# Kernel tuning notes

Measured on AMD Instinct MI355X. Metric: run time of the kernel, lower is better.

## Reference

```python
import jax, jax.numpy as jnp
import numpy as np

B, T, D = 8, 2048, 512
F = 512          # filters (== D due to residual add)
K = 7            # kernel_size
H = 128          # hidden_dim of kernel generator (hard-coded in source)
LN_EPS = 1e-3    # keras LayerNormalization default epsilon


def setup_inputs() -> dict:
    key = jax.random.key(0)
    ks = jax.random.split(key, 8)
    x = jax.random.normal(ks[0], (B, T, D), dtype=jnp.float32)
    # kernel generator: Dense(D->H, relu) then Dense(H->K*F)
    W1 = jax.random.normal(ks[1], (D, H), dtype=jnp.float32) * (1.0 / np.sqrt(D))
    b1 = jnp.zeros((H,), dtype=jnp.float32)
    W2 = jax.random.normal(ks[2], (H, K * F), dtype=jnp.float32) * (1.0 / np.sqrt(H))
    b2 = jnp.zeros((K * F,), dtype=jnp.float32)
    # LayerNorm params
    gamma = jnp.ones((F,), dtype=jnp.float32)
    beta = jnp.zeros((F,), dtype=jnp.float32)
    return {"x": x, "W1": W1, "b1": b1, "W2": W2, "b2": b2,
            "gamma": gamma, "beta": beta}


def _dynamic_conv_block(x, W1, b1, W2, b2, gamma, beta):
    # per-token dynamic kernels: [B, T, K, F]
    h = jax.nn.relu(jnp.einsum("btd,dh->bth", x, W1) + b1)
    kernels = (jnp.einsum("bth,hf->btf", h, W2) + b2).reshape(B, T, K, F)
    # extract sliding-window patches (same padding): [B, T, K, D]
    pad = K // 2
    xp = jnp.pad(x, ((0, 0), (pad, pad), (0, 0)))
    patches = jnp.stack([xp[:, i:i + T, :] for i in range(K)], axis=2)
    # per-token conv: contract over window K and input channels D
    conv_out = jnp.einsum("btkd,btkf->btf", patches, kernels)
    # residual + LayerNorm + relu (dropout is identity at inference)
    y = conv_out + x
    mu = jnp.mean(y, axis=-1, keepdims=True)
    var = jnp.mean(jnp.square(y - mu), axis=-1, keepdims=True)
    y = (y - mu) * jax.lax.rsqrt(var + LN_EPS) * gamma + beta
    return jax.nn.relu(y)


def reference(x, W1, b1, W2, b2, gamma, beta):
    return _dynamic_conv_block(x, W1, b1, W2, b2, gamma, beta)
```

## Files before the change

### kernel.cpp

```cpp
#include <hip/hip_runtime.h>

#define NT 2048
#define ND 512
#define NH 128
#define NKW 7
#define KP 960

typedef float f32x4 __attribute__((ext_vector_type(4)));
typedef __bf16 bf16x8 __attribute__((ext_vector_type(8)));
typedef unsigned short u16;
typedef unsigned int u32;
typedef u16 u16x8 __attribute__((ext_vector_type(8)));

__device__ __forceinline__ u16 f2bf(float f){
  u32 u = __builtin_bit_cast(u32, f);
  return (u16)((u + 0x7fffu + ((u>>16)&1u)) >> 16);
}
__device__ __forceinline__ float bf2f(u16 s){
  u32 u = ((u32)s)<<16;
  return __builtin_bit_cast(float, u);
}
__device__ __forceinline__ void store16_lds(void* p, const u16 u[8]){
  u32 d0 = (u32)u[0] | ((u32)u[1]<<16);
  u32 d1 = (u32)u[2] | ((u32)u[3]<<16);
  u32 d2 = (u32)u[4] | ((u32)u[5]<<16);
  u32 d3 = (u32)u[6] | ((u32)u[7]<<16);
  int4 vv; vv.x=(int)d0; vv.y=(int)d1; vv.z=(int)d2; vv.w=(int)d3;
  *(int4*)p = vv;
}

__global__ __launch_bounds__(256) void prep_kernel(
    const float* __restrict__ W1, const float* __restrict__ W2,
    const float* __restrict__ b2, u16* __restrict__ W1T, u16* __restrict__ B2T)
{
  __shared__ float T[64][65];
  const int b = blockIdx.x, tid = threadIdx.x;
  if (b < 16){
    const int d0 = (b>>1)*64, h0 = (b&1)*64;
    #pragma unroll
    for (int r=0;r<16;++r){
      int idx=r*256+tid; int dl=idx>>6, hl=idx&63;
      T[dl][hl] = W1[(size_t)(d0+dl)*NH + h0+hl];
    }
    __syncthreads();
    #pragma unroll
    for (int r=0;r<16;++r){
      int idx=r*256+tid; int hl=idx>>6, dl=idx&63;
      W1T[(size_t)(h0+hl)*ND + d0+dl] = f2bf(T[dl][hl]);
    }
  } else if (b < 128){
    const int bb = b-16;
    const int h0 = (bb&1)*64, c0 = (bb>>1)*64;
    #pragma unroll
    for (int r=0;r<16;++r){
      int idx=r*256+tid; int hl=idx>>6, cl=idx&63;
      T[hl][cl] = W2[(size_t)(h0+hl)*(NKW*ND) + c0+cl];
    }
    __syncthreads();
    #pragma unroll
    for (int r=0;r<16;++r){
      int idx=r*256+tid; int cl=idx>>6, hl=idx&63;
      int c = c0+cl; int n = c & (ND-1), k = c >> 9;
      B2T[(size_t)n*KP + k*NH + h0+hl] = f2bf(T[hl][cl]);
    }
  } else {
    const int bb = b-128;
    #pragma unroll
    for (int r=0;r<16;++r){
      int idx = bb*4096 + r*256 + tid;
      int n = idx>>6, j = idx&63;
      B2T[(size_t)n*KP + 896 + j] = (j<NKW)? f2bf(b2[(size_t)j*ND+n]) : (u16)0;
    }
  }
}

__device__ __forceinline__ void loadB2(const char* B2T, int kc, int w, int l,
                                       bf16x8 (*bf)[4]){
  #pragma unroll
  for (int kk=0;kk<2;++kk)
    #pragma unroll
    for (int ni=0;ni<4;++ni){
      int rowB = w*64 + ni*16 + (l&15);
      bf[kk][ni] = *(const bf16x8*)(B2T + (size_t)rowB*(KP*2) + kc*128 + kk*64 + (l>>4)*16);
    }
}
__device__ __forceinline__ void loadB1(const char* W1T, int kc, int w, int l,
                                       bf16x8 (*bf)[2]){
  #pragma unroll
  for (int kk=0;kk<2;++kk)
    #pragma unroll
    for (int ni=0;ni<2;++ni){
      int rowB = w*32 + ni*16 + (l&15);
      bf[kk][ni] = *(const bf16x8*)(W1T + (size_t)rowB*(ND*2) + kc*128 + kk*64 + (l>>4)*16);
    }
}

__global__ __launch_bounds__(256,2) void gemm1_kernel(
    const float* __restrict__ x, const u16* __restrict__ W1T,
    const float* __restrict__ b1, u16* __restrict__ hout, float* __restrict__ rs)
{
  __shared__ __align__(16) u16 At[2][32*64];
  const int tid = threadIdx.x, w = tid>>6, l = tid&63;
  const int m_base = blockIdx.x*32;
  const int row = tid>>3, slot = tid&7;
  const float* xrow = x + (size_t)(m_base+row)*ND + slot*8;
  float rsum = 0.f;
  f32x4 acc[2][2] = {};
  bf16x8 bufA[2][2], bufB[2][2];

  auto stageA = [&](u16* dst, const float4& p0, const float4& p1){
    rsum += (p0.x+p0.y)+(p0.z+p0.w)+((p1.x+p1.y)+(p1.z+p1.w));
    u16 u[8] = {f2bf(p0.x),f2bf(p0.y),f2bf(p0.z),f2bf(p0.w),
                f2bf(p1.x),f2bf(p1.y),f2bf(p1.z),f2bf(p1.w)};
    int byte = row*128 + ((slot*16) ^ ((row&7)<<4));
    store16_lds((char*)dst + byte, u);
  };

  float4 c0 = *(const float4*)(xrow);
  float4 c1 = *(const float4*)(xrow+4);
  loadB1((const char*)W1T, 0, w, l, bufA);
  stageA(At[0], c0, c1);
  __syncthreads();

  #pragma unroll
  for (int kc=0;kc<8;++kc){
    bf16x8 (*bc)[2] = (kc&1)? bufB : bufA;
    bf16x8 (*bn)[2] = (kc&1)? bufA : bufB;
    float4 n0, n1;
    if (kc<7){
      n0 = *(const float4*)(xrow + (kc+1)*64);
      n1 = *(const float4*)(xrow + (kc+1)*64 + 4);
      loadB1((const char*)W1T, kc+1, w, l, bn);
    }
    const char* curA = (const char*)At[kc&1];
    #pragma unroll
    for (int kk=0;kk<2;++kk){
      bf16x8 af[2];
      #pragma unroll
      for (int mi=0;mi<2;++mi){
        int r2 = mi*16 + (l&15);
        int byte = r2*128 + (((kk*64)+((l>>4)*16)) ^ ((r2&7)<<4));
        af[mi] = *(const bf16x8*)(curA + byte);
      }
      #pragma unroll
      for (int mi=0;mi<2;++mi)
        #pragma unroll
        for (int ni=0;ni<2;++ni)
          acc[mi][ni] = __builtin_amdgcn_mfma_f32_16x16x32_bf16(af[mi], bc[kk][ni], acc[mi][ni],0,0,0);
    }
    if (kc<7){
      stageA(At[(kc&1)^1], n0, n1);
      __syncthreads();
    }
  }
  rsum += __shfl_xor(rsum,1);
  rsum += __shfl_xor(rsum,2);
  rsum += __shfl_xor(rsum,4);
  if ((tid&7)==0) rs[m_base+row] = rsum;
  #pragma unroll
  for (int ni=0;ni<2;++ni){
    int n = w*32 + ni*16 + (l&15);
    float bias = b1[n];
    #pragma unroll
    for (int mi=0;mi<2;++mi){
      #pragma unroll
      for (int r=0;r<4;++r){
        int m = mi*16 + (l>>4)*4 + r;
        float v = fmaxf(acc[mi][ni][r] + bias, 0.f);
        hout[(size_t)(m_base+m)*NH + n] = f2bf(v);
      }
    }
  }
}

__global__ __launch_bounds__(512,2) void gemm2_kernel(
    const float* __restrict__ x, const u16* __restrict__ hbuf,
    const u16* __restrict__ B2T, const float* __restrict__ rs,
    const float* __restrict__ gamma, const float* __restrict__ beta,
    float* __restrict__ out)
{
  __shared__ __align__(16) u16 At[2][64*64];
  __shared__ float s_lds[64][8];
  __shared__ float red_s[64][8], red_q[64][8];
  __shared__ float mu_lds[64], rstd_lds[64];

  const int tid = threadIdx.x, w = tid>>6, l = tid&63;
  const int m_base = blockIdx.x*64;
  const int row = tid>>3, slot = tid&7;

  {
    int rr = tid>>3, k = tid&7;
    float v = 0.f;
    if (k < NKW){
      int tg = m_base + rr;
      int ti = tg & (NT-1);
      int idx = ti + k - 3;
      if (idx >= 0 && idx < NT) v = rs[(tg & ~(NT-1)) + idx];
    }
    s_lds[rr][k] = v;
  }
  u16x8 hv_e = *(const u16x8*)(hbuf + (size_t)(m_base+row)*NH + slot*8);
  u16x8 hv_o = *(const u16x8*)(hbuf + (size_t)(m_base+row)*NH + 64 + slot*8);

  bf16x8 bufA[2][4], bufB[2][4];
  loadB2((const char*)B2T, 0, w, l, bufA);

  auto stageA = [&](u16* dst, int kc2){
    u16 u[8];
    if (kc2 < 14){
      float sv = s_lds[row][kc2>>1];
      u16x8 hv = (kc2&1)? hv_o : hv_e;
      #pragma unroll
      for (int j=0;j<8;++j) u[j] = f2bf(bf2f(hv[j])*sv);
    } else {
      #pragma unroll
      for (int j=0;j<8;++j){
        int e2 = slot*8+j;
        u[j] = (e2<NKW)? f2bf(s_lds[row][e2]) : (u16)0;
      }
    }
    int byte = row*128 + ((slot*16) ^ ((row&7)<<4));
    store16_lds((char*)dst + byte, u);
  };

  __syncthreads();
  stageA(At[0], 0);
  __syncthreads();

  f32x4 acc[4][4] = {};
  #pragma unroll
  for (int kc=0;kc<15;++kc){
    bf16x8 (*bc)[4] = (kc&1)? bufB : bufA;
    bf16x8 (*bn)[4] = (kc&1)? bufA : bufB;
    if (kc<14) loadB2((const char*)B2T, kc+1, w, l, bn);
    const char* curA = (const char*)At[kc&1];
    #pragma unroll
    for (int kk=0;kk<2;++kk){
      bf16x8 af[4];
      #pragma unroll
      for (int mi=0;mi<4;++mi){
        int r2 = mi*16 + (l&15);
        int byte = r2*128 + (((kk*64)+((l>>4)*16)) ^ ((r2&7)<<4));
        af[mi] = *(const bf16x8*)(curA + byte);
      }
      #pragma unroll
      for (int mi=0;mi<4;++mi)
        #pragma unroll
        for (int ni=0;ni<4;++ni)
          acc[mi][ni] = __builtin_amdgcn_mfma_f32_16x16x32_bf16(af[mi], bc[kk][ni], acc[mi][ni],0,0,0);
    }
    if (kc<14){
      stageA(At[(kc&1)^1], kc+1);
      __syncthreads();
    }
  }

  #pragma unroll
  for (int mi=0;mi<4;++mi){
    #pragma unroll
    for (int r=0;r<4;++r){
      int m = mi*16 + (l>>4)*4 + r;
      int tg = m_base + m;
      float ps=0.f, pq=0.f;
      #pragma unroll
      for (int ni=0;ni<4;++ni){
        int n = w*64 + ni*16 + (l&15);
        float v = acc[mi][ni][r] + x[(size_t)tg*ND + n];
        acc[mi][ni][r] = v;
        ps += v; pq += v*v;
      }
      #pragma unroll
      for (int msk=1; msk<16; msk<<=1){ ps += __shfl_xor(ps,msk); pq += __shfl_xor(pq,msk); }
      if ((l&15)==0){ red_s[m][w]=ps; red_q[m][w]=pq; }
    }
  }
  __syncthreads();
  if (tid < 64){
    float ssum=0.f, sq=0.f;
    #pragma unroll
    for (int ww=0; ww<8; ++ww){ ssum += red_s[tid][ww]; sq += red_q[tid][ww]; }
    float mu = ssum * (1.0f/ND);
    float var = sq*(1.0f/ND) - mu*mu;
    mu_lds[tid] = mu;
    rstd_lds[tid] = rsqrtf(var + 1e-3f);
  }
  __syncthreads();
  float gv[4], bv[4];
  #pragma unroll
  for (int ni=0;ni<4;++ni){
    int n = w*64 + ni*16 + (l&15);
    gv[ni] = gamma[n]; bv[ni] = beta[n];
  }
  #pragma unroll
  for (int mi=0;mi<4;++mi){
    #pragma unroll
    for (int r=0;r<4;++r){
      int m = mi*16 + (l>>4)*4 + r;
      int tg = m_base + m;
      float mu = mu_lds[m], rstd = rstd_lds[m];
      #pragma unroll
      for (int ni=0;ni<4;++ni){
        int n = w*64 + ni*16 + (l&15);
        float v = (acc[mi][ni][r]-mu)*rstd*gv[ni] + bv[ni];
        out[(size_t)tg*ND + n] = fmaxf(v, 0.f);
      }
    }
  }
}

extern "C" void kernel_launch(void* const* d_in, const int* in_sizes, int n_in,
                              void* d_out, int out_size, void* d_ws, size_t ws_size,
                              hipStream_t stream)
{
  (void)in_sizes; (void)n_in; (void)out_size; (void)ws_size;
  const float* x     = (const float*)d_in[0];
  const float* W1    = (const float*)d_in[1];
  const float* b1    = (const float*)d_in[2];
  const float* W2    = (const float*)d_in[3];
  const float* b2    = (const float*)d_in[4];
  const float* gamma = (const float*)d_in[5];
  const float* beta  = (const float*)d_in[6];
  float* out = (float*)d_out;

  char* ws = (char*)d_ws;
  u16*   W1T  = (u16*)(ws);
  u16*   B2T  = (u16*)(ws + 131072);
  float* rs   = (float*)(ws + 131072 + 983040);
  u16*   hbuf = (u16*)(ws + 131072 + 983040 + 65536);

  prep_kernel<<<136, 256, 0, stream>>>(W1, W2, b2, W1T, B2T);
  gemm1_kernel<<<512, 256, 0, stream>>>(x, W1T, b1, hbuf, rs);
  gemm2_kernel<<<256, 512, 0, stream>>>(x, hbuf, B2T, rs, gamma, beta, out);
}
```

Measured before the change: 142.1 us.

## Fuse hidden-layer GEMM into dynamic-conv GEMM kernel via LDS staging

Merges the first GEMM (x·W1 with relu) and the row-sum computation into the second GEMM kernel. Each block stages its 64 bf16 x rows in LDS, computes h locally into LDS, and computes halo row sums directly. This removes a kernel launch and the global round trip of h and row sums. It adds a scheduling barrier after the B prefetch. The cost is much larger LDS use, which may reduce occupancy, plus extra halo reads.

```diff
diff --git a/kernel.cpp b/kernel.cpp
--- a/kernel.cpp
+++ b/kernel.cpp
@@ -5,6 +5,7 @@
 #define NH 128
 #define NKW 7
 #define KP 960
+#define NTOK 16384
 
 typedef float f32x4 __attribute__((ext_vector_type(4)));
 typedef __bf16 bf16x8 __attribute__((ext_vector_type(8)));
@@ -19,6 +20,12 @@
 __device__ __forceinline__ float bf2f(u16 s){
   u32 u = ((u32)s)<<16;
   return __builtin_bit_cast(float, u);
+}
+__device__ __forceinline__ bf16x8 pack8(const float4& a, const float4& b){
+  u16x8 u;
+  u[0]=f2bf(a.x); u[1]=f2bf(a.y); u[2]=f2bf(a.z); u[3]=f2bf(a.w);
+  u[4]=f2bf(b.x); u[5]=f2bf(b.y); u[6]=f2bf(b.z); u[7]=f2bf(b.w);
+  return __builtin_bit_cast(bf16x8, u);
 }
 __device__ __forceinline__ void store16_lds(void* p, const u16 u[8]){
   u32 d0 = (u32)u[0] | ((u32)u[1]<<16);
@@ -74,142 +81,122 @@
   }
 }
 
-__device__ __forceinline__ void loadB2(const char* B2T, int kc, int w, int l,
-                                       bf16x8 (*bf)[4]){
-  #pragma unroll
-  for (int kk=0;kk<2;++kk)
-    #pragma unroll
-    for (int ni=0;ni<4;++ni){
-      int rowB = w*64 + ni*16 + (l&15);
-      bf[kk][ni] = *(const bf16x8*)(B2T + (size_t)rowB*(KP*2) + kc*128 + kk*64 + (l>>4)*16);
-    }
-}
-__device__ __forceinline__ void loadB1(const char* W1T, int kc, int w, int l,
-                                       bf16x8 (*bf)[2]){
-  #pragma unroll
-  for (int kk=0;kk<2;++kk)
-    #pragma unroll
-    for (int ni=0;ni<2;++ni){
-      int rowB = w*32 + ni*16 + (l&15);
-      bf[kk][ni] = *(const bf16x8*)(W1T + (size_t)rowB*(ND*2) + kc*128 + kk*64 + (l>>4)*16);
-    }
-}
-
-__global__ __launch_bounds__(256,2) void gemm1_kernel(
+__global__ __launch_bounds__(512,2) void fused_kernel(
     const float* __restrict__ x, const u16* __restrict__ W1T,
-    const float* __restrict__ b1, u16* __restrict__ hout, float* __restrict__ rs)
-{
-  __shared__ __align__(16) u16 At[2][32*64];
-  const int tid = threadIdx.x, w = tid>>6, l = tid&63;
-  const int m_base = blockIdx.x*32;
-  const int row = tid>>3, slot = tid&7;
-  const float* xrow = x + (size_t)(m_base+row)*ND + slot*8;
-  float rsum = 0.f;
-  f32x4 acc[2][2] = {};
-  bf16x8 bufA[2][2], bufB[2][2];
-
-  auto stageA = [&](u16* dst, const float4& p0, const float4& p1){
-    rsum += (p0.x+p0.y)+(p0.z+p0.w)+((p1.x+p1.y)+(p1.z+p1.w));
-    u16 u[8] = {f2bf(p0.x),f2bf(p0.y),f2bf(p0.z),f2bf(p0.w),
-                f2bf(p1.x),f2bf(p1.y),f2bf(p1.z),f2bf(p1.w)};
-    int byte = row*128 + ((slot*16) ^ ((row&7)<<4));
-    store16_lds((char*)dst + byte, u);
-  };
-
-  float4 c0 = *(const float4*)(xrow);
-  float4 c1 = *(const float4*)(xrow+4);
-  loadB1((const char*)W1T, 0, w, l, bufA);
-  stageA(At[0], c0, c1);
-  __syncthreads();
-
-  #pragma unroll
-  for (int kc=0;kc<8;++kc){
-    bf16x8 (*bc)[2] = (kc&1)? bufB : bufA;
-    bf16x8 (*bn)[2] = (kc&1)? bufA : bufB;
-    float4 n0, n1;
-    if (kc<7){
-      n0 = *(const float4*)(xrow + (kc+1)*64);
-      n1 = *(const float4*)(xrow + (kc+1)*64 + 4);
-      loadB1((const char*)W1T, kc+1, w, l, bn);
-    }
-    const char* curA = (const char*)At[kc&1];
-    #pragma unroll
-    for (int kk=0;kk<2;++kk){
-      bf16x8 af[2];
-      #pragma unroll
-      for (int mi=0;mi<2;++mi){
-        int r2 = mi*16 + (l&15);
-        int byte = r2*128 + (((kk*64)+((l>>4)*16)) ^ ((r2&7)<<4));
-        af[mi] = *(const bf16x8*)(curA + byte);
-      }
-      #pragma unroll
-      for (int mi=0;mi<2;++mi)
-        #pragma unroll
-        for (int ni=0;ni<2;++ni)
-          acc[mi][ni] = __builtin_amdgcn_mfma_f32_16x16x32_bf16(af[mi], bc[kk][ni], acc[mi][ni],0,0,0);
-    }
-    if (kc<7){
-      stageA(At[(kc&1)^1], n0, n1);
-      __syncthreads();
-    }
-  }
-  rsum += __shfl_xor(rsum,1);
-  rsum += __shfl_xor(rsum,2);
-  rsum += __shfl_xor(rsum,4);
-  if ((tid&7)==0) rs[m_base+row] = rsum;
-  #pragma unroll
-  for (int ni=0;ni<2;++ni){
-    int n = w*32 + ni*16 + (l&15);
-    float bias = b1[n];
-    #pragma unroll
-    for (int mi=0;mi<2;++mi){
-      #pragma unroll
-      for (int r=0;r<4;++r){
-        int m = mi*16 + (l>>4)*4 + r;
-        float v = fmaxf(acc[mi][ni][r] + bias, 0.f);
-        hout[(size_t)(m_base+m)*NH + n] = f2bf(v);
-      }
-    }
-  }
-}
-
-__global__ __launch_bounds__(512,2) void gemm2_kernel(
-    const float* __restrict__ x, const u16* __restrict__ hbuf,
-    const u16* __restrict__ B2T, const float* __restrict__ rs,
+    const float* __restrict__ b1, const u16* __restrict__ B2T,
     const float* __restrict__ gamma, const float* __restrict__ beta,
     float* __restrict__ out)
 {
+  __shared__ __align__(16) u16 xb_lds[64*512];
+  __shared__ __align__(16) u16 h_lds[64*128];
   __shared__ __align__(16) u16 At[2][64*64];
+  __shared__ float rs_lds[70];
   __shared__ float s_lds[64][8];
   __shared__ float red_s[64][8], red_q[64][8];
   __shared__ float mu_lds[64], rstd_lds[64];
 
   const int tid = threadIdx.x, w = tid>>6, l = tid&63;
   const int m_base = blockIdx.x*64;
-  const int row = tid>>3, slot = tid&7;
-
+
+  {
+    const int r = tid>>3, slot = tid&7;
+    const float4* p = (const float4*)(x + (size_t)(m_base+r)*ND + slot*64);
+    float s = 0.f;
+    #pragma unroll
+    for (int i=0;i<8;++i){
+      float4 a = p[2*i], b2v = p[2*i+1];
+      s += (a.x+a.y)+(a.z+a.w) + (b2v.x+b2v.y)+(b2v.z+b2v.w);
+      u16 u[8] = {f2bf(a.x),f2bf(a.y),f2bf(a.z),f2bf(a.w),
+                  f2bf(b2v.x),f2bf(b2v.y),f2bf(b2v.z),f2bf(b2v.w)};
+      int byte = r*1024 + ((slot*128 + i*16) ^ ((r&7)<<4));
+      store16_lds((char*)xb_lds + byte, u);
+    }
+    s += __shfl_xor(s,1); s += __shfl_xor(s,2); s += __shfl_xor(s,4);
+    if (slot==0) rs_lds[3+r] = s;
+    if (l < 8 && w < 6){
+      int j = (w<3)? w : w+64;
+      int tg2 = m_base + j - 3;
+      float s2 = 0.f;
+      if (tg2 >= 0 && tg2 < NTOK){
+        const float4* p2 = (const float4*)(x + (size_t)tg2*ND + l*64);
+        #pragma unroll
+        for (int i=0;i<16;++i){ float4 v = p2[i]; s2 += (v.x+v.y)+(v.z+v.w); }
+      }
+      s2 += __shfl_xor(s2,1); s2 += __shfl_xor(s2,2); s2 += __shfl_xor(s2,4);
+      if (l==0) rs_lds[j] = s2;
+    }
+  }
+  __syncthreads();
   {
     int rr = tid>>3, k = tid&7;
     float v = 0.f;
     if (k < NKW){
-      int tg = m_base + rr;
-      int ti = tg & (NT-1);
+      int ti = (m_base+rr) & (NT-1);
       int idx = ti + k - 3;
-      if (idx >= 0 && idx < NT) v = rs[(tg & ~(NT-1)) + idx];
+      if (idx >= 0 && idx < NT) v = rs_lds[rr+k];
     }
     s_lds[rr][k] = v;
   }
-  u16x8 hv_e = *(const u16x8*)(hbuf + (size_t)(m_base+row)*NH + slot*8);
-  u16x8 hv_o = *(const u16x8*)(hbuf + (size_t)(m_base+row)*NH + 64 + slot*8);
-
+
+  {
+    const int wm = w>>2, wn = w&3;
+    f32x4 acc1[2][2] = {};
+    const u16* bbase = W1T + (size_t)(wn*32 + (l&15))*ND + (l>>4)*8;
+    #pragma unroll
+    for (int kc=0;kc<16;++kc){
+      bf16x8 af[2], bfr[2];
+      #pragma unroll
+      for (int mi=0;mi<2;++mi){
+        int rr = wm*32 + mi*16 + (l&15);
+        int byte = rr*1024 + ((kc*64 + (l>>4)*16) ^ ((rr&7)<<4));
+        af[mi] = *(const bf16x8*)((const char*)xb_lds + byte);
+      }
+      #pragma unroll
+      for (int ni=0;ni<2;++ni)
+        bfr[ni] = *(const bf16x8*)(bbase + (size_t)ni*16*ND + kc*32);
+      #pragma unroll
+      for (int mi=0;mi<2;++mi)
+        #pragma unroll
+        for (int ni=0;ni<2;++ni)
+          acc1[mi][ni] = __builtin_amdgcn_mfma_f32_16x16x32_bf16(af[mi], bfr[ni], acc1[mi][ni],0,0,0);
+    }
+    #pragma unroll
+    for (int ni=0;ni<2;++ni){
+      int col = wn*32 + ni*16 + (l&15);
+      float bias = b1[col];
+      #pragma unroll
+      for (int mi=0;mi<2;++mi){
+        #pragma unroll
+        for (int r=0;r<4;++r){
+          int row = wm*32 + mi*16 + (l>>4)*4 + r;
+          float v = fmaxf(acc1[mi][ni][r] + bias, 0.f);
+          int byte = row*256 + ((2*col) ^ ((row&7)<<4));
+          *(u16*)((char*)h_lds + byte) = f2bf(v);
+        }
+      }
+    }
+  }
+  __syncthreads();
+
+  f32x4 acc[4][4] = {};
   bf16x8 bufA[2][4], bufB[2][4];
-  loadB2((const char*)B2T, 0, w, l, bufA);
-
+  const int row = tid>>3, slot = tid&7;
+
+  auto loadB = [&](int kc, bf16x8 (*bf)[4]){
+    #pragma unroll
+    for (int kk=0;kk<2;++kk)
+      #pragma unroll
+      for (int ni=0;ni<4;++ni){
+        int rowB = w*64 + ni*16 + (l&15);
+        bf[kk][ni] = *(const bf16x8*)((const char*)B2T + (size_t)rowB*(KP*2) + kc*128 + kk*64 + (l>>4)*16);
+      }
+  };
   auto stageA = [&](u16* dst, int kc2){
     u16 u[8];
     if (kc2 < 14){
       float sv = s_lds[row][kc2>>1];
-      u16x8 hv = (kc2&1)? hv_o : hv_e;
+      const char* src = (const char*)h_lds + row*256 + (((kc2&1)*128 + slot*16) ^ ((row&7)<<4));
+      u16x8 hv = *(const u16x8*)src;
       #pragma unroll
       for (int j=0;j<8;++j) u[j] = f2bf(bf2f(hv[j])*sv);
     } else {
@@ -223,16 +210,18 @@
     store16_lds((char*)dst + byte, u);
   };
 
-  __syncthreads();
+  loadB(0, bufA);
   stageA(At[0], 0);
   __syncthreads();
 
-  f32x4 acc[4][4] = {};
   #pragma unroll
   for (int kc=0;kc<15;++kc){
     bf16x8 (*bc)[4] = (kc&1)? bufB : bufA;
     bf16x8 (*bn)[4] = (kc&1)? bufA : bufB;
-    if (kc<14) loadB2((const char*)B2T, kc+1, w, l, bn);
+    if (kc<14){
+      loadB(kc+1, bn);
+      __builtin_amdgcn_sched_barrier(0);
+    }
     const char* curA = (const char*)At[kc&1];
     #pragma unroll
     for (int kk=0;kk<2;++kk){
@@ -323,12 +312,9 @@
   float* out = (float*)d_out;
 
   char* ws = (char*)d_ws;
-  u16*   W1T  = (u16*)(ws);
-  u16*   B2T  = (u16*)(ws + 131072);
-  float* rs   = (float*)(ws + 131072 + 983040);
-  u16*   hbuf = (u16*)(ws + 131072 + 983040 + 65536);
+  u16* W1T = (u16*)(ws);
+  u16* B2T = (u16*)(ws + 131072);
 
   prep_kernel<<<136, 256, 0, stream>>>(W1, W2, b2, W1T, B2T);
-  gemm1_kernel<<<512, 256, 0, stream>>>(x, W1T, b1, hbuf, rs);
-  gemm2_kernel<<<256, 512, 0, stream>>>(x, hbuf, B2T, rs, gamma, beta, out);
-}
+  fused_kernel<<<256, 512, 0, stream>>>(x, W1T, b1, B2T, gamma, beta, out);
+}
```

New measurement: 144.2 us. About the same (+1.5%).
